# Kernel optimization log

Hardware: AMD Instinct MI355X
Metric: run time of the kernel (lower is better)

Reference implementation:

```python
import jax, jax.numpy as jnp
import numpy as np

N, F, HD, E, K, T, IDX = 50000, 128, 256, 800000, 3, 7, 0


def setup_inputs() -> dict:
    key = jax.random.key(0)
    ks = jax.random.split(key, 18)
    s = 0.05  # param init scale
    return {
        "x": jax.random.normal(ks[0], (N, F), jnp.float32),
        "edge_index": jax.random.randint(ks[1], (2, E), 0, N),
        "edge_weight": jax.random.uniform(ks[2], (E,), jnp.float32),
        "h": jax.random.normal(ks[3], (N, HD), jnp.float32),
        "c": jax.random.normal(ks[4], (N, HD), jnp.float32),
        # 4 ChebConvs on X and 4 on H (gates i, f, c, o), each with K Chebyshev weights
        "theta_x": jax.random.normal(ks[5], (4, K, F, HD), jnp.float32) * s,
        "bias_x": jnp.zeros((4, HD), jnp.float32),
        "theta_h": jax.random.normal(ks[6], (4, K, HD, HD), jnp.float32) * s,
        "bias_h": jnp.zeros((4, HD), jnp.float32),
        "w_c": jax.random.normal(ks[7], (3, HD), jnp.float32) * s,  # peephole w_c_i, w_c_f, w_c_o
        "b_gate": jnp.zeros((4, HD), jnp.float32),  # b_i, b_f, b_c, b_o
        # decoder LSTM (input_size=1, hidden=HD), torch gate order i, f, g, o
        "w_ih": jax.random.normal(ks[8], (4 * HD, 1), jnp.float32) * s,
        "w_hh": jax.random.normal(ks[9], (4 * HD, HD), jnp.float32) * s,
        "b_ih": jnp.zeros((4 * HD,), jnp.float32),
        "b_hh": jnp.zeros((4 * HD,), jnp.float32),
        "w_out": jax.random.normal(ks[10], (1, HD), jnp.float32) * s,
        "b_out": jnp.zeros((1,), jnp.float32),
    }


def _cheb_stack(feat, src, dst, w_norm):
    """Stacked Chebyshev bases [K, N, d]; L_hat = -A_norm (sym norm, lambda_max=2)."""
    def lhat(v):
        msg = w_norm[:, None] * v[src]              # [E, d] gather
        return -jax.ops.segment_sum(msg, dst, num_segments=N)  # scatter-add
    Tx = [feat]
    if K > 1:
        Tx.append(lhat(feat))
    for _ in range(2, K):
        Tx.append(2.0 * lhat(Tx[-1]) - Tx[-2])
    return jnp.stack(Tx)


def reference(x, edge_index, edge_weight, h, c, theta_x, bias_x, theta_h, bias_h,
              w_c, b_gate, w_ih, w_hh, b_ih, b_hh, w_out, b_out):
    src, dst = edge_index[0], edge_index[1]
    # ChebConv.__norm__: remove self loops, sym-normalized Laplacian, scale by 2/lambda_max=1,
    # add -I -> L_hat off-diag = -w_norm, diag = 0
    w = jnp.where(src == dst, 0.0, edge_weight)
    deg = jax.ops.segment_sum(w, src, num_segments=N)
    dis = jnp.where(deg > 0, jax.lax.rsqrt(jnp.maximum(deg, 1e-20)), 0.0)
    w_norm = dis[src] * w * dis[dst]

    # GConvLSTM encode: one conv per gate on X and on H; bases shared across gates
    gx = jnp.einsum('knf,gkfo->gno', _cheb_stack(x, src, dst, w_norm), theta_x) + bias_x[:, None, :]
    gh = jnp.einsum('knf,gkfo->gno', _cheb_stack(h, src, dst, w_norm), theta_h) + bias_h[:, None, :]
    g = gx + gh  # [4, N, HD] gates i, f, c, o
    I = jax.nn.sigmoid(g[0] + w_c[0] * c + b_gate[0])
    Fg = jax.nn.sigmoid(g[1] + w_c[1] * c + b_gate[1])
    Cn = Fg * c + I * jnp.tanh(g[2] + b_gate[2])
    O = jax.nn.sigmoid(g[3] + w_c[2] * Cn + b_gate[3])
    Hn = O * jnp.tanh(Cn)

    h0 = Hn[IDX:IDX + 1]          # [1, HD]
    c0 = Cn[IDX:IDX + 1]
    inp0 = x[IDX, -1:][None]      # [1, 1]

    def step(carry, _):
        hd, cd, inp = carry
        gates = inp @ w_ih.T + hd @ w_hh.T + b_ih + b_hh  # [1, 4*HD]
        i, f, gg, o = jnp.split(gates, 4, axis=1)
        cn = jax.nn.sigmoid(f) * cd + jax.nn.sigmoid(i) * jnp.tanh(gg)
        hn = jax.nn.sigmoid(o) * jnp.tanh(cn)
        out = hn @ w_out.T + b_out                         # [1, 1]
        return (hn, cn, out), out

    _, outs = jax.lax.scan(step, (h0, c0, inp0), None, length=T)  # [T, 1, 1]
    prediction = outs[:, :, 0]  # squeeze dim 2 -> [T, 1]
    return prediction
```

## Files before the change

kernel.cpp:

```cpp
#include <hip/hip_runtime.h>
#include <math.h>

#define NN 50000
#define FD 128
#define HDIM 256
#define NE 800000
#define NBR_CAP 512
#define M_CAP 8192
#define TT 7
#define TPB 256
#define GB 96
#define PSLICE 12
#define GRP 21
#define ECHUNK 2048
#define SBLK 32
#define FGRID (GB + SBLK)
#define SPIN_CAP 50000000

#define O_NBRCNT   0
#define O_MCNT     64
#define O_GDONE    128
#define O_HSYNC    512
#define O_DEG      16896
#define O_BITMAP   216896
#define O_ZERO_END 223168
#define O_NBRNODE  223168
#define O_NBRW     225216
#define O_MS       227264
#define O_MD       260032
#define O_MW       292800
#define O_GPART    325568

__device__ __forceinline__ float sigm(float v) { return 1.f / (1.f + expf(-v)); }
__device__ __forceinline__ float dis_of(float dg) {
    return dg > 0.f ? rsqrtf(fmaxf(dg, 1e-20f)) : 0.f;
}
__device__ __forceinline__ float slf(const float* p) {
    return __hip_atomic_load(p, __ATOMIC_RELAXED, __HIP_MEMORY_SCOPE_SYSTEM);
}
__device__ __forceinline__ void ssf(float* p, float v) {
    __hip_atomic_store(p, v, __ATOMIC_RELAXED, __HIP_MEMORY_SCOPE_SYSTEM);
}

__global__ void k_nbr(const int* __restrict__ ei, const float* __restrict__ ew,
                      char* __restrict__ ws) {
    int*   nbrCnt = (int*)(ws + O_NBRCNT);
    int*   nbrNode= (int*)(ws + O_NBRNODE);
    float* nbrW   = (float*)(ws + O_NBRW);

    int gid = blockIdx.x * blockDim.x + threadIdx.x;
    if (gid < (O_ZERO_END - O_MCNT) / 4) ((unsigned*)(ws + O_MCNT))[gid] = 0u;

    int e0 = gid * 4;
    if (e0 >= NE) return;
    int4 d4 = *(const int4*)&ei[NE + e0];
    float4 w4 = *(const float4*)&ew[e0];
    int dd[4] = {d4.x, d4.y, d4.z, d4.w};
    float wv[4] = {w4.x, w4.y, w4.z, w4.w};
    #pragma unroll
    for (int k = 0; k < 4; ++k) {
        if (dd[k] == 0 && wv[k] != 0.f) {
            int s = ei[e0 + k];
            if (s != 0) {
                int slot = atomicAdd(nbrCnt, 1);
                if (slot < NBR_CAP) { nbrNode[slot] = s; nbrW[slot] = wv[k]; }
            }
        }
    }
}

__global__ void k_match(const int* __restrict__ ei, const float* __restrict__ ew,
                        char* __restrict__ ws) {
    const int* nbrCnt = (const int*)(ws + O_NBRCNT);
    const int* nbrNode= (const int*)(ws + O_NBRNODE);
    int*      mCnt   = (int*)(ws + O_MCNT);
    int*      mS     = (int*)(ws + O_MS);
    int*      mD     = (int*)(ws + O_MD);
    float*    mW     = (float*)(ws + O_MW);
    unsigned* bitmap = (unsigned*)(ws + O_BITMAP);

    __shared__ int sNode[NBR_CAP];
    __shared__ int sCnt;
    if (threadIdx.x == 0) sCnt = min(*nbrCnt, NBR_CAP);
    __syncthreads();
    int cnt = sCnt;
    for (int i = threadIdx.x; i < cnt; i += blockDim.x) sNode[i] = nbrNode[i];
    __syncthreads();
    if (blockIdx.x == 0 && threadIdx.x == 0) atomicOr(&bitmap[0], 1u);

    int i = blockIdx.x * blockDim.x + threadIdx.x;
    int e0 = i * 4;
    if (e0 >= NE) return;
    int4 s4 = *(const int4*)&ei[e0];
    int4 d4 = *(const int4*)&ei[NE + e0];
    float4 w4 = *(const float4*)&ew[e0];
    int ss[4] = {s4.x, s4.y, s4.z, s4.w};
    int dd[4] = {d4.x, d4.y, d4.z, d4.w};
    float wv[4] = {w4.x, w4.y, w4.z, w4.w};
    bool m[4];
    #pragma unroll
    for (int k = 0; k < 4; ++k) m[k] = (dd[k] == 0);
    for (int j = 0; j < cnt; ++j) {
        int nv = sNode[j];
        #pragma unroll
        for (int k = 0; k < 4; ++k) m[k] |= (dd[k] == nv);
    }
    #pragma unroll
    for (int k = 0; k < 4; ++k) {
        int s = ss[k], d = dd[k];
        float w = wv[k];
        if (s == d || w == 0.f || !m[k]) continue;
        int slot = atomicAdd(mCnt, 1);
        if (slot < M_CAP) { mS[slot] = s; mD[slot] = d; mW[slot] = w; }
        atomicOr(&bitmap[s >> 5], 1u << (s & 31));
        atomicOr(&bitmap[d >> 5], 1u << (d & 31));
    }
}

__global__ void k_deg(const int* __restrict__ ei, const float* __restrict__ ew,
                      char* __restrict__ ws) {
    const unsigned* bitmap = (const unsigned*)(ws + O_BITMAP);
    float* deg = (float*)(ws + O_DEG);
    int i = blockIdx.x * blockDim.x + threadIdx.x;
    int e0 = i * 4;
    if (e0 >= NE) return;
    int4 s4 = *(const int4*)&ei[e0];
    int4 d4 = *(const int4*)&ei[NE + e0];
    float4 w4 = *(const float4*)&ew[e0];
    int ss[4] = {s4.x, s4.y, s4.z, s4.w};
    int dd[4] = {d4.x, d4.y, d4.z, d4.w};
    float wv[4] = {w4.x, w4.y, w4.z, w4.w};
    #pragma unroll
    for (int k = 0; k < 4; ++k) {
        int s = ss[k];
        if (s == dd[k] || wv[k] == 0.f) continue;
        if (bitmap[s >> 5] & (1u << (s & 31)))
            atomicAdd(&deg[s], wv[k]);
    }
}

__global__ __launch_bounds__(TPB) void k_fused(
    const float* __restrict__ x, const float* __restrict__ h, const float* __restrict__ c,
    const float* __restrict__ theta_x, const float* __restrict__ bias_x,
    const float* __restrict__ theta_h, const float* __restrict__ bias_h,
    const float* __restrict__ w_c, const float* __restrict__ b_gate,
    const float* __restrict__ w_ih, const float* __restrict__ w_hh,
    const float* __restrict__ b_ih, const float* __restrict__ b_hh,
    const float* __restrict__ w_out, const float* __restrict__ b_out,
    float* __restrict__ out, char* __restrict__ ws) {

    const float*        deg    = (const float*)(ws + O_DEG);
    const int*          nbrCnt = (const int*)(ws + O_NBRCNT);
    const int*          mCnt   = (const int*)(ws + O_MCNT);
    const int*          nbrNode= (const int*)(ws + O_NBRNODE);
    const float*        nbrW   = (const float*)(ws + O_NBRW);
    const int*          mS     = (const int*)(ws + O_MS);
    const int*          mD     = (const int*)(ws + O_MD);
    const float*        mW     = (const float*)(ws + O_MW);
    float*              gpart  = (float*)(ws + O_GPART);
    unsigned*           gdone  = (unsigned*)(ws + O_GDONE);
    unsigned long long* hsync  = (unsigned long long*)(ws + O_HSYNC);

    __shared__ int   sNode[NBR_CAP];
    __shared__ float sWl[NBR_CAP];
    __shared__ float cf1[ECHUNK], cf2[ECHUNK];
    __shared__ int   sS[ECHUNK];
    __shared__ float tp1[GRP][PSLICE], tp2[GRP][PSLICE];
    __shared__ float tslice[PSLICE];
    __shared__ __align__(16) float sh[HDIM];
    __shared__ float sdot[32];
    __shared__ float swsum[4];
    __shared__ int   sCnt, sMcnt;

    const int tid = threadIdx.x, bid = blockIdx.x;

    if (bid < GB) {
        if (tid == 0) { sCnt = min(*nbrCnt, NBR_CAP); sMcnt = min(*mCnt, M_CAP); }
        __syncthreads();
        const int ncnt = sCnt, mcnt = sMcnt;
        for (int i = tid; i < ncnt; i += TPB) { sNode[i] = nbrNode[i]; sWl[i] = nbrW[i]; }
        __syncthreads();

        const bool isx = bid < 32;
        const int qstart = bid * PSLICE - (isx ? 0 : 3 * FD);
        const float* fb0 = isx ? x : h;
        const int fstride = isx ? FD : HDIM;

        const int pl = tid % PSLICE, gr = tid / PSLICE;
        const float* fbase = fb0 + (qstart + pl) % fstride;
        const float dis0 = dis_of(deg[0]);

        float a1 = 0.f, a2 = 0.f;
        for (int c0i = 0; c0i < mcnt; c0i += ECHUNK) {
            int clen = min(ECHUNK, mcnt - c0i);
            for (int i = tid; i < clen; i += TPB) {
                int sI = mS[c0i + i], dI = mD[c0i + i];
                float w = mW[c0i + i];
                float disd = dis_of(deg[dI]);
                float wn = dis_of(deg[sI]) * w * disd;
                float Wd = 0.f;
                for (int j = 0; j < ncnt; ++j) Wd += (sNode[j] == dI) ? sWl[j] : 0.f;
                cf1[i] = (dI == 0) ? wn : 0.f;
                cf2[i] = wn * (dis0 * disd * Wd);
                sS[i] = sI;
            }
            __syncthreads();
            if (gr < GRP) {
                int i = gr;
                for (; i + 3 * GRP < clen; i += 4 * GRP) {
                    int s0 = sS[i], s1 = sS[i + GRP], s2 = sS[i + 2 * GRP], s3 = sS[i + 3 * GRP];
                    float c10 = cf1[i], c11 = cf1[i + GRP], c12 = cf1[i + 2 * GRP], c13 = cf1[i + 3 * GRP];
                    float c20 = cf2[i], c21 = cf2[i + GRP], c22 = cf2[i + 2 * GRP], c23 = cf2[i + 3 * GRP];
                    float v0 = fbase[(size_t)s0 * fstride];
                    float v1 = fbase[(size_t)s1 * fstride];
                    float v2 = fbase[(size_t)s2 * fstride];
                    float v3 = fbase[(size_t)s3 * fstride];
                    a1 += c10 * v0 + c11 * v1 + c12 * v2 + c13 * v3;
                    a2 += c20 * v0 + c21 * v1 + c22 * v2 + c23 * v3;
                }
                for (; i < clen; i += GRP) {
                    float v = fbase[(size_t)sS[i] * fstride];
                    a1 += cf1[i] * v;
                    a2 += cf2[i] * v;
                }
            }
            __syncthreads();
        }
        if (gr < GRP) { tp1[gr][pl] = a1; tp2[gr][pl] = a2; }
        __syncthreads();
        if (tid < PSLICE) {
            float A1 = 0.f, A2 = 0.f;
            #pragma unroll
            for (int g2 = 0; g2 < GRP; ++g2) { A1 += tp1[g2][tid]; A2 += tp2[g2][tid]; }
            int q = qstart + tid;
            int ko = q / fstride;
            float ff0 = fb0[q % fstride];
            tslice[tid] = (ko == 0) ? ff0 : ((ko == 1) ? -A1 : 2.f * A2 - ff0);
        }
        __syncthreads();

        {
            const float* tb = isx ? theta_x : theta_h;
            const size_t gs = isx ? (size_t)(3 * FD) * HDIM : (size_t)(3 * HDIM) * HDIM;
            float g0 = 0.f, g1 = 0.f, g2v = 0.f, g3 = 0.f;
            #pragma unroll
            for (int pp = 0; pp < PSLICE; ++pp) {
                float tv = tslice[pp];
                const float* row = tb + (size_t)(qstart + pp) * HDIM;
                g0  += tv * row[tid];
                g1  += tv * row[gs + tid];
                g2v += tv * row[2 * gs + tid];
                g3  += tv * row[3 * gs + tid];
            }
            float* gp = gpart + (size_t)bid * 1024;
            ssf(&gp[tid], g0);
            ssf(&gp[HDIM + tid], g1);
            ssf(&gp[2 * HDIM + tid], g2v);
            ssf(&gp[3 * HDIM + tid], g3);
        }
        __syncthreads();
        if (tid == 0)
            __hip_atomic_store(&gdone[bid], 1u, __ATOMIC_RELEASE, __HIP_MEMORY_SCOPE_SYSTEM);
        return;
    }

    const int sbid = bid - GB;

    const int rl = tid >> 3, seg = tid & 7;
    const int grow = (rl >> 3) * HDIM + sbid * 8 + (rl & 7);
    float4 wreg[8];
    #pragma unroll
    for (int k = 0; k < 8; ++k)
        wreg[k] = *(const float4*)&w_hh[(size_t)grow * HDIM + seg * 32 + k * 4];
    const float wih_r = w_ih[grow];
    const float br    = b_ih[grow] + b_hh[grow];
    const float bo    = b_out[0];
    const float wout_r = w_out[tid];

    if (tid < GB) {
        int sp = 0;
        while (__hip_atomic_load(&gdone[tid], __ATOMIC_RELAXED,
                                 __HIP_MEMORY_SCOPE_SYSTEM) == 0u) {
            if (++sp > SPIN_CAP) break;
        }
    }
    __syncthreads();

    {
        const int d = tid >> 3, j = tid & 7;
        const int g = d >> 3, kk = d & 7, o = sbid * 8 + kk;
        float s = 0.f;
        #pragma unroll
        for (int pb = j; pb < GB; pb += 8) s += slf(&gpart[(size_t)pb * 1024 + g * HDIM + o]);
        s += __shfl_down(s, 4);
        s += __shfl_down(s, 2);
        s += __shfl_down(s, 1);
        if (j == 0) sdot[d] = s;
    }
    __syncthreads();

    float creg = 0.f;
    if (tid < 8) {
        const int o = sbid * 8 + tid;
        float g0 = sdot[tid]      + bias_x[o]            + bias_h[o];
        float g1 = sdot[8 + tid]  + bias_x[HDIM + o]     + bias_h[HDIM + o];
        float g2 = sdot[16 + tid] + bias_x[2 * HDIM + o] + bias_h[2 * HDIM + o];
        float g3 = sdot[24 + tid] + bias_x[3 * HDIM + o] + bias_h[3 * HDIM + o];
        float c0 = c[o];
        float I  = sigm(g0 + w_c[o] * c0 + b_gate[o]);
        float Fg = sigm(g1 + w_c[HDIM + o] * c0 + b_gate[HDIM + o]);
        float Cn = Fg * c0 + I * tanhf(g2 + b_gate[2 * HDIM + o]);
        float O  = sigm(g3 + w_c[2 * HDIM + o] * Cn + b_gate[3 * HDIM + o]);
        float h0 = O * tanhf(Cn);
        creg = Cn;
        unsigned long long pk = (1ull << 32) | (unsigned long long)__float_as_uint(h0);
        __hip_atomic_store(&hsync[o], pk, __ATOMIC_RELAXED, __HIP_MEMORY_SCOPE_SYSTEM);
    }
    {
        unsigned long long v;
        int sp = 0;
        do {
            v = __hip_atomic_load(&hsync[tid], __ATOMIC_RELAXED, __HIP_MEMORY_SCOPE_SYSTEM);
            if ((unsigned)(v >> 32) == 1u) break;
        } while (++sp < SPIN_CAP);
        sh[tid] = __uint_as_float((unsigned)v);
    }
    __syncthreads();
    float sinp = x[FD - 1];

    for (int t = 0; t < TT; ++t) {
        float acc = 0.f;
        const float* shh = &sh[seg * 32];
        #pragma unroll
        for (int k = 0; k < 8; ++k) {
            float4 hv = *(const float4*)&shh[k * 4];
            acc += hv.x * wreg[k].x + hv.y * wreg[k].y + hv.z * wreg[k].z + hv.w * wreg[k].w;
        }
        acc += __shfl_down(acc, 4);
        acc += __shfl_down(acc, 2);
        acc += __shfl_down(acc, 1);
        if (seg == 0) sdot[rl] = acc + sinp * wih_r + br;
        __syncthreads();
        if (tid < 8) {
            float iv = sdot[tid], fv = sdot[8 + tid], gv = sdot[16 + tid], ov = sdot[24 + tid];
            float cn = sigm(fv) * creg + sigm(iv) * tanhf(gv);
            float hn = sigm(ov) * tanhf(cn);
            creg = cn;
            unsigned long long pk = (((unsigned long long)(t + 2)) << 32)
                                  | (unsigned long long)__float_as_uint(hn);
            __hip_atomic_store(&hsync[(t + 1) * HDIM + sbid * 8 + tid], pk,
                               __ATOMIC_RELAXED, __HIP_MEMORY_SCOPE_SYSTEM);
        }
        float hval;
        {
            unsigned long long v;
            int sp = 0;
            do {
                v = __hip_atomic_load(&hsync[(t + 1) * HDIM + tid],
                                      __ATOMIC_RELAXED, __HIP_MEMORY_SCOPE_SYSTEM);
                if ((unsigned)(v >> 32) == (unsigned)(t + 2)) break;
            } while (++sp < SPIN_CAP);
            hval = __uint_as_float((unsigned)v);
        }
        sh[tid] = hval;
        float pw = wout_r * hval;
        pw += __shfl_down(pw, 32);
        pw += __shfl_down(pw, 16);
        pw += __shfl_down(pw, 8);
        pw += __shfl_down(pw, 4);
        pw += __shfl_down(pw, 2);
        pw += __shfl_down(pw, 1);
        if ((tid & 63) == 0) swsum[tid >> 6] = pw;
        __syncthreads();
        float sval = swsum[0] + swsum[1] + swsum[2] + swsum[3] + bo;
        sinp = sval;
        if (sbid == 0 && tid == 0) out[t] = sval;
    }
}

extern "C" void kernel_launch(void* const* d_in, const int* in_sizes, int n_in,
                              void* d_out, int out_size, void* d_ws, size_t ws_size,
                              hipStream_t stream) {
    const float* x       = (const float*)d_in[0];
    const int*   ei      = (const int*)d_in[1];
    const float* ew      = (const float*)d_in[2];
    const float* h       = (const float*)d_in[3];
    const float* c       = (const float*)d_in[4];
    const float* theta_x = (const float*)d_in[5];
    const float* bias_x  = (const float*)d_in[6];
    const float* theta_h = (const float*)d_in[7];
    const float* bias_h  = (const float*)d_in[8];
    const float* w_c     = (const float*)d_in[9];
    const float* b_gate  = (const float*)d_in[10];
    const float* w_ih    = (const float*)d_in[11];
    const float* w_hh    = (const float*)d_in[12];
    const float* b_ih    = (const float*)d_in[13];
    const float* b_hh    = (const float*)d_in[14];
    const float* w_out   = (const float*)d_in[15];
    const float* b_out   = (const float*)d_in[16];
    char* ws = (char*)d_ws;
    float* out = (float*)d_out;

    hipMemsetAsync(ws, 0, 64, stream);

    int eb4 = (NE / 4 + TPB - 1) / TPB;
    k_nbr<<<eb4, TPB, 0, stream>>>(ei, ew, ws);
    k_match<<<eb4, TPB, 0, stream>>>(ei, ew, ws);
    k_deg<<<eb4, TPB, 0, stream>>>(ei, ew, ws);
    k_fused<<<FGRID, TPB, 0, stream>>>(x, h, c, theta_x, bias_x, theta_h, bias_h,
                                       w_c, b_gate, w_ih, w_hh, b_ih, b_hh,
                                       w_out, b_out, out, ws);
}
```

Measured before the change: 53.62 us.

## Replace in-kernel spin-synchronized LSTM decode with per-step kernel launches

The autoregressive decoder no longer runs inside the fused kernel with cross-block spin-waits on tagged hsync values. The fused kernel now writes the initial h and c to workspace buffers, and a separate small kernel is launched for each of the seven decode steps, followed by a final kernel for the last output. Kernel boundaries replace the global flag polling, removing atomic spinning and the risk of blocks that are not co-resident. The cost is eight extra launches and w_hh being reloaded from memory on every step instead of staying in registers.

```diff
diff --git a/kernel.cpp b/kernel.cpp
--- a/kernel.cpp
+++ b/kernel.cpp
@@ -15,21 +15,23 @@
 #define ECHUNK 2048
 #define SBLK 32
 #define FGRID (GB + SBLK)
+#define SB 32
 #define SPIN_CAP 50000000
 
 #define O_NBRCNT   0
 #define O_MCNT     64
 #define O_GDONE    128
-#define O_HSYNC    512
-#define O_DEG      16896
-#define O_BITMAP   216896
-#define O_ZERO_END 223168
-#define O_NBRNODE  223168
-#define O_NBRW     225216
-#define O_MS       227264
-#define O_MD       260032
-#define O_MW       292800
-#define O_GPART    325568
+#define O_DEG      512
+#define O_BITMAP   200512
+#define O_ZERO_END 206784
+#define O_NBRNODE  206784
+#define O_NBRW     208832
+#define O_MS       210880
+#define O_MD       243648
+#define O_MW       276416
+#define O_GPART    309184
+#define O_HBUF     702400
+#define O_CBUF     710592
 
 __device__ __forceinline__ float sigm(float v) { return 1.f / (1.f + expf(-v)); }
 __device__ __forceinline__ float dis_of(float dg) {
@@ -144,22 +146,20 @@
     const float* __restrict__ theta_x, const float* __restrict__ bias_x,
     const float* __restrict__ theta_h, const float* __restrict__ bias_h,
     const float* __restrict__ w_c, const float* __restrict__ b_gate,
-    const float* __restrict__ w_ih, const float* __restrict__ w_hh,
-    const float* __restrict__ b_ih, const float* __restrict__ b_hh,
-    const float* __restrict__ w_out, const float* __restrict__ b_out,
-    float* __restrict__ out, char* __restrict__ ws) {
-
-    const float*        deg    = (const float*)(ws + O_DEG);
-    const int*          nbrCnt = (const int*)(ws + O_NBRCNT);
-    const int*          mCnt   = (const int*)(ws + O_MCNT);
-    const int*          nbrNode= (const int*)(ws + O_NBRNODE);
-    const float*        nbrW   = (const float*)(ws + O_NBRW);
-    const int*          mS     = (const int*)(ws + O_MS);
-    const int*          mD     = (const int*)(ws + O_MD);
-    const float*        mW     = (const float*)(ws + O_MW);
-    float*              gpart  = (float*)(ws + O_GPART);
-    unsigned*           gdone  = (unsigned*)(ws + O_GDONE);
-    unsigned long long* hsync  = (unsigned long long*)(ws + O_HSYNC);
+    char* __restrict__ ws) {
+
+    const float*  deg    = (const float*)(ws + O_DEG);
+    const int*    nbrCnt = (const int*)(ws + O_NBRCNT);
+    const int*    mCnt   = (const int*)(ws + O_MCNT);
+    const int*    nbrNode= (const int*)(ws + O_NBRNODE);
+    const float*  nbrW   = (const float*)(ws + O_NBRW);
+    const int*    mS     = (const int*)(ws + O_MS);
+    const int*    mD     = (const int*)(ws + O_MD);
+    const float*  mW     = (const float*)(ws + O_MW);
+    float*        gpart  = (float*)(ws + O_GPART);
+    unsigned*     gdone  = (unsigned*)(ws + O_GDONE);
+    float*        hbuf   = (float*)(ws + O_HBUF);
+    float*        cbuf   = (float*)(ws + O_CBUF);
 
     __shared__ int   sNode[NBR_CAP];
     __shared__ float sWl[NBR_CAP];
@@ -167,9 +167,7 @@
     __shared__ int   sS[ECHUNK];
     __shared__ float tp1[GRP][PSLICE], tp2[GRP][PSLICE];
     __shared__ float tslice[PSLICE];
-    __shared__ __align__(16) float sh[HDIM];
     __shared__ float sdot[32];
-    __shared__ float swsum[4];
     __shared__ int   sCnt, sMcnt;
 
     const int tid = threadIdx.x, bid = blockIdx.x;
@@ -266,17 +264,6 @@
 
     const int sbid = bid - GB;
 
-    const int rl = tid >> 3, seg = tid & 7;
-    const int grow = (rl >> 3) * HDIM + sbid * 8 + (rl & 7);
-    float4 wreg[8];
-    #pragma unroll
-    for (int k = 0; k < 8; ++k)
-        wreg[k] = *(const float4*)&w_hh[(size_t)grow * HDIM + seg * 32 + k * 4];
-    const float wih_r = w_ih[grow];
-    const float br    = b_ih[grow] + b_hh[grow];
-    const float bo    = b_out[0];
-    const float wout_r = w_out[tid];
-
     if (tid < GB) {
         int sp = 0;
         while (__hip_atomic_load(&gdone[tid], __ATOMIC_RELAXED,
@@ -299,7 +286,6 @@
     }
     __syncthreads();
 
-    float creg = 0.f;
     if (tid < 8) {
         const int o = sbid * 8 + tid;
         float g0 = sdot[tid]      + bias_x[o]            + bias_h[o];
@@ -311,71 +297,86 @@
         float Fg = sigm(g1 + w_c[HDIM + o] * c0 + b_gate[HDIM + o]);
         float Cn = Fg * c0 + I * tanhf(g2 + b_gate[2 * HDIM + o]);
         float O  = sigm(g3 + w_c[2 * HDIM + o] * Cn + b_gate[3 * HDIM + o]);
-        float h0 = O * tanhf(Cn);
-        creg = Cn;
-        unsigned long long pk = (1ull << 32) | (unsigned long long)__float_as_uint(h0);
-        __hip_atomic_store(&hsync[o], pk, __ATOMIC_RELAXED, __HIP_MEMORY_SCOPE_SYSTEM);
-    }
-    {
-        unsigned long long v;
-        int sp = 0;
-        do {
-            v = __hip_atomic_load(&hsync[tid], __ATOMIC_RELAXED, __HIP_MEMORY_SCOPE_SYSTEM);
-            if ((unsigned)(v >> 32) == 1u) break;
-        } while (++sp < SPIN_CAP);
-        sh[tid] = __uint_as_float((unsigned)v);
-    }
-    __syncthreads();
-    float sinp = x[FD - 1];
-
-    for (int t = 0; t < TT; ++t) {
-        float acc = 0.f;
-        const float* shh = &sh[seg * 32];
-        #pragma unroll
-        for (int k = 0; k < 8; ++k) {
-            float4 hv = *(const float4*)&shh[k * 4];
-            acc += hv.x * wreg[k].x + hv.y * wreg[k].y + hv.z * wreg[k].z + hv.w * wreg[k].w;
-        }
-        acc += __shfl_down(acc, 4);
-        acc += __shfl_down(acc, 2);
-        acc += __shfl_down(acc, 1);
-        if (seg == 0) sdot[rl] = acc + sinp * wih_r + br;
-        __syncthreads();
-        if (tid < 8) {
-            float iv = sdot[tid], fv = sdot[8 + tid], gv = sdot[16 + tid], ov = sdot[24 + tid];
-            float cn = sigm(fv) * creg + sigm(iv) * tanhf(gv);
-            float hn = sigm(ov) * tanhf(cn);
-            creg = cn;
-            unsigned long long pk = (((unsigned long long)(t + 2)) << 32)
-                                  | (unsigned long long)__float_as_uint(hn);
-            __hip_atomic_store(&hsync[(t + 1) * HDIM + sbid * 8 + tid], pk,
-                               __ATOMIC_RELAXED, __HIP_MEMORY_SCOPE_SYSTEM);
-        }
-        float hval;
-        {
-            unsigned long long v;
-            int sp = 0;
-            do {
-                v = __hip_atomic_load(&hsync[(t + 1) * HDIM + tid],
-                                      __ATOMIC_RELAXED, __HIP_MEMORY_SCOPE_SYSTEM);
-                if ((unsigned)(v >> 32) == (unsigned)(t + 2)) break;
-            } while (++sp < SPIN_CAP);
-            hval = __uint_as_float((unsigned)v);
-        }
-        sh[tid] = hval;
-        float pw = wout_r * hval;
-        pw += __shfl_down(pw, 32);
-        pw += __shfl_down(pw, 16);
-        pw += __shfl_down(pw, 8);
-        pw += __shfl_down(pw, 4);
-        pw += __shfl_down(pw, 2);
-        pw += __shfl_down(pw, 1);
-        if ((tid & 63) == 0) swsum[tid >> 6] = pw;
-        __syncthreads();
-        float sval = swsum[0] + swsum[1] + swsum[2] + swsum[3] + bo;
-        sinp = sval;
-        if (sbid == 0 && tid == 0) out[t] = sval;
-    }
+        hbuf[o] = O * tanhf(Cn);
+        cbuf[o] = Cn;
+    }
+}
+
+__global__ __launch_bounds__(TPB) void k_step(
+    int t, const float* __restrict__ x,
+    const float* __restrict__ w_ih, const float* __restrict__ w_hh,
+    const float* __restrict__ b_ih, const float* __restrict__ b_hh,
+    const float* __restrict__ w_out, const float* __restrict__ b_out,
+    float* __restrict__ out, char* __restrict__ ws) {
+
+    float* hbuf = (float*)(ws + O_HBUF);
+    float* cbuf = (float*)(ws + O_CBUF);
+
+    __shared__ __align__(16) float sh[HDIM];
+    __shared__ float sdot[32];
+    __shared__ float swsum[4];
+
+    const int tid = threadIdx.x, bid = blockIdx.x;
+    const float* hr = hbuf + t * HDIM;
+
+    float hv = hr[tid];
+    sh[tid] = hv;
+    float pw = hv * w_out[tid];
+    pw += __shfl_down(pw, 32);
+    pw += __shfl_down(pw, 16);
+    pw += __shfl_down(pw, 8);
+    pw += __shfl_down(pw, 4);
+    pw += __shfl_down(pw, 2);
+    pw += __shfl_down(pw, 1);
+    if ((tid & 63) == 0) swsum[tid >> 6] = pw;
+    __syncthreads();
+    const float bo = b_out[0];
+    const float sval = swsum[0] + swsum[1] + swsum[2] + swsum[3] + bo;
+    const float sinp = (t == 0) ? x[FD - 1] : sval;
+    if (t > 0 && bid == 0 && tid == 0) out[t - 1] = sval;
+
+    const int rl = tid >> 3, seg = tid & 7;
+    const int grow = (rl >> 3) * HDIM + bid * 8 + (rl & 7);
+    const float* wrow = w_hh + (size_t)grow * HDIM + seg * 32;
+    const float* shh = &sh[seg * 32];
+    float acc = 0.f;
+    #pragma unroll
+    for (int k = 0; k < 8; ++k) {
+        float4 wv = *(const float4*)&wrow[k * 4];
+        float4 hv4 = *(const float4*)&shh[k * 4];
+        acc += hv4.x * wv.x + hv4.y * wv.y + hv4.z * wv.z + hv4.w * wv.w;
+    }
+    acc += __shfl_down(acc, 4);
+    acc += __shfl_down(acc, 2);
+    acc += __shfl_down(acc, 1);
+    if (seg == 0) sdot[rl] = acc + sinp * w_ih[grow] + b_ih[grow] + b_hh[grow];
+    __syncthreads();
+
+    if (tid < 8) {
+        const int dim = bid * 8 + tid;
+        float cd = cbuf[t * HDIM + dim];
+        float iv = sdot[tid], fv = sdot[8 + tid], gv = sdot[16 + tid], ov = sdot[24 + tid];
+        float cn = sigm(fv) * cd + sigm(iv) * tanhf(gv);
+        float hn = sigm(ov) * tanhf(cn);
+        hbuf[(t + 1) * HDIM + dim] = hn;
+        cbuf[(t + 1) * HDIM + dim] = cn;
+    }
+}
+
+__global__ void k_fin(const float* __restrict__ w_out, const float* __restrict__ b_out,
+                      float* __restrict__ out, char* __restrict__ ws) {
+    const float* hr = (const float*)(ws + O_HBUF) + TT * HDIM;
+    const int tid = threadIdx.x;
+    float pw = 0.f;
+    #pragma unroll
+    for (int j = 0; j < 4; ++j) pw += hr[tid * 4 + j] * w_out[tid * 4 + j];
+    pw += __shfl_down(pw, 32);
+    pw += __shfl_down(pw, 16);
+    pw += __shfl_down(pw, 8);
+    pw += __shfl_down(pw, 4);
+    pw += __shfl_down(pw, 2);
+    pw += __shfl_down(pw, 1);
+    if (tid == 0) out[TT - 1] = pw + b_out[0];
 }
 
 extern "C" void kernel_launch(void* const* d_in, const int* in_sizes, int n_in,
@@ -408,6 +409,8 @@
     k_match<<<eb4, TPB, 0, stream>>>(ei, ew, ws);
     k_deg<<<eb4, TPB, 0, stream>>>(ei, ew, ws);
     k_fused<<<FGRID, TPB, 0, stream>>>(x, h, c, theta_x, bias_x, theta_h, bias_h,
-                                       w_c, b_gate, w_ih, w_hh, b_ih, b_hh,
-                                       w_out, b_out, out, ws);
-}
+                                       w_c, b_gate, ws);
+    for (int t = 0; t < TT; ++t)
+        k_step<<<SB, TPB, 0, stream>>>(t, x, w_ih, w_hh, b_ih, b_hh, w_out, b_out, out, ws);
+    k_fin<<<1, 64, 0, stream>>>(w_out, b_out, out, ws);
+}
```

New measurement: 66.62 us. 1.24x slower.

## Split decoder LSTM tail into separate kernel, replacing initial hsync handoff

Applied to the files above, without the earlier changes.

The autoregressive decoder is moved out of the fused kernel into a new k_tail2 launch of 32 blocks. The fused kernel now writes the initial h and c state to global buffers instead of publishing h through the spin-synchronised hsync slots. This drops one cross-block spin barrier and the w_hh register preload from the fused kernel, so those blocks finish sooner. In exchange it adds a kernel launch boundary, and the tail can no longer preload its weights while the gate-partial blocks are still working.

```diff
diff --git a/kernel.cpp b/kernel.cpp
--- a/kernel.cpp
+++ b/kernel.cpp
@@ -15,31 +15,34 @@
 #define ECHUNK 2048
 #define SBLK 32
 #define FGRID (GB + SBLK)
+#define SB 32
 #define SPIN_CAP 50000000
 
 #define O_NBRCNT   0
 #define O_MCNT     64
 #define O_GDONE    128
 #define O_HSYNC    512
-#define O_DEG      16896
-#define O_BITMAP   216896
-#define O_ZERO_END 223168
-#define O_NBRNODE  223168
-#define O_NBRW     225216
-#define O_MS       227264
-#define O_MD       260032
-#define O_MW       292800
-#define O_GPART    325568
+#define O_HBUF     16896
+#define O_CBUF     17920
+#define O_DEG      18944
+#define O_BITMAP   218944
+#define O_ZERO_END 225216
+#define O_NBRNODE  225216
+#define O_NBRW     227264
+#define O_MS       229312
+#define O_MD       262080
+#define O_MW       294848
+#define O_GPART    327616
 
 __device__ __forceinline__ float sigm(float v) { return 1.f / (1.f + expf(-v)); }
 __device__ __forceinline__ float dis_of(float dg) {
     return dg > 0.f ? rsqrtf(fmaxf(dg, 1e-20f)) : 0.f;
 }
+__device__ __forceinline__ void ssf(float* p, float v) {
+    __hip_atomic_store(p, v, __ATOMIC_RELAXED, __HIP_MEMORY_SCOPE_SYSTEM);
+}
 __device__ __forceinline__ float slf(const float* p) {
     return __hip_atomic_load(p, __ATOMIC_RELAXED, __HIP_MEMORY_SCOPE_SYSTEM);
-}
-__device__ __forceinline__ void ssf(float* p, float v) {
-    __hip_atomic_store(p, v, __ATOMIC_RELAXED, __HIP_MEMORY_SCOPE_SYSTEM);
 }
 
 __global__ void k_nbr(const int* __restrict__ ei, const float* __restrict__ ew,
@@ -144,22 +147,20 @@
     const float* __restrict__ theta_x, const float* __restrict__ bias_x,
     const float* __restrict__ theta_h, const float* __restrict__ bias_h,
     const float* __restrict__ w_c, const float* __restrict__ b_gate,
-    const float* __restrict__ w_ih, const float* __restrict__ w_hh,
-    const float* __restrict__ b_ih, const float* __restrict__ b_hh,
-    const float* __restrict__ w_out, const float* __restrict__ b_out,
-    float* __restrict__ out, char* __restrict__ ws) {
-
-    const float*        deg    = (const float*)(ws + O_DEG);
-    const int*          nbrCnt = (const int*)(ws + O_NBRCNT);
-    const int*          mCnt   = (const int*)(ws + O_MCNT);
-    const int*          nbrNode= (const int*)(ws + O_NBRNODE);
-    const float*        nbrW   = (const float*)(ws + O_NBRW);
-    const int*          mS     = (const int*)(ws + O_MS);
-    const int*          mD     = (const int*)(ws + O_MD);
-    const float*        mW     = (const float*)(ws + O_MW);
-    float*              gpart  = (float*)(ws + O_GPART);
-    unsigned*           gdone  = (unsigned*)(ws + O_GDONE);
-    unsigned long long* hsync  = (unsigned long long*)(ws + O_HSYNC);
+    char* __restrict__ ws) {
+
+    const float*  deg    = (const float*)(ws + O_DEG);
+    const int*    nbrCnt = (const int*)(ws + O_NBRCNT);
+    const int*    mCnt   = (const int*)(ws + O_MCNT);
+    const int*    nbrNode= (const int*)(ws + O_NBRNODE);
+    const float*  nbrW   = (const float*)(ws + O_NBRW);
+    const int*    mS     = (const int*)(ws + O_MS);
+    const int*    mD     = (const int*)(ws + O_MD);
+    const float*  mW     = (const float*)(ws + O_MW);
+    float*        gpart  = (float*)(ws + O_GPART);
+    unsigned*     gdone  = (unsigned*)(ws + O_GDONE);
+    float*        hbuf   = (float*)(ws + O_HBUF);
+    float*        cbuf   = (float*)(ws + O_CBUF);
 
     __shared__ int   sNode[NBR_CAP];
     __shared__ float sWl[NBR_CAP];
@@ -167,9 +168,7 @@
     __shared__ int   sS[ECHUNK];
     __shared__ float tp1[GRP][PSLICE], tp2[GRP][PSLICE];
     __shared__ float tslice[PSLICE];
-    __shared__ __align__(16) float sh[HDIM];
     __shared__ float sdot[32];
-    __shared__ float swsum[4];
     __shared__ int   sCnt, sMcnt;
 
     const int tid = threadIdx.x, bid = blockIdx.x;
@@ -266,17 +265,6 @@
 
     const int sbid = bid - GB;
 
-    const int rl = tid >> 3, seg = tid & 7;
-    const int grow = (rl >> 3) * HDIM + sbid * 8 + (rl & 7);
-    float4 wreg[8];
-    #pragma unroll
-    for (int k = 0; k < 8; ++k)
-        wreg[k] = *(const float4*)&w_hh[(size_t)grow * HDIM + seg * 32 + k * 4];
-    const float wih_r = w_ih[grow];
-    const float br    = b_ih[grow] + b_hh[grow];
-    const float bo    = b_out[0];
-    const float wout_r = w_out[tid];
-
     if (tid < GB) {
         int sp = 0;
         while (__hip_atomic_load(&gdone[tid], __ATOMIC_RELAXED,
@@ -299,7 +287,6 @@
     }
     __syncthreads();
 
-    float creg = 0.f;
     if (tid < 8) {
         const int o = sbid * 8 + tid;
         float g0 = sdot[tid]      + bias_x[o]            + bias_h[o];
@@ -311,20 +298,41 @@
         float Fg = sigm(g1 + w_c[HDIM + o] * c0 + b_gate[HDIM + o]);
         float Cn = Fg * c0 + I * tanhf(g2 + b_gate[2 * HDIM + o]);
         float O  = sigm(g3 + w_c[2 * HDIM + o] * Cn + b_gate[3 * HDIM + o]);
-        float h0 = O * tanhf(Cn);
-        creg = Cn;
-        unsigned long long pk = (1ull << 32) | (unsigned long long)__float_as_uint(h0);
-        __hip_atomic_store(&hsync[o], pk, __ATOMIC_RELAXED, __HIP_MEMORY_SCOPE_SYSTEM);
-    }
-    {
-        unsigned long long v;
-        int sp = 0;
-        do {
-            v = __hip_atomic_load(&hsync[tid], __ATOMIC_RELAXED, __HIP_MEMORY_SCOPE_SYSTEM);
-            if ((unsigned)(v >> 32) == 1u) break;
-        } while (++sp < SPIN_CAP);
-        sh[tid] = __uint_as_float((unsigned)v);
-    }
+        hbuf[o] = O * tanhf(Cn);
+        cbuf[o] = Cn;
+    }
+}
+
+__global__ __launch_bounds__(TPB) void k_tail2(
+    const float* __restrict__ x,
+    const float* __restrict__ w_ih, const float* __restrict__ w_hh,
+    const float* __restrict__ b_ih, const float* __restrict__ b_hh,
+    const float* __restrict__ w_out, const float* __restrict__ b_out,
+    float* __restrict__ out, char* __restrict__ ws) {
+
+    unsigned long long* hsync = (unsigned long long*)(ws + O_HSYNC);
+    const float* hbuf = (const float*)(ws + O_HBUF);
+    const float* cbuf = (const float*)(ws + O_CBUF);
+
+    __shared__ __align__(16) float sh[HDIM];
+    __shared__ float sdot[32];
+    __shared__ float swsum[4];
+
+    const int tid = threadIdx.x, bid = blockIdx.x;
+
+    const int rl = tid >> 3, seg = tid & 7;
+    const int grow = (rl >> 3) * HDIM + bid * 8 + (rl & 7);
+    float4 wreg[8];
+    #pragma unroll
+    for (int k = 0; k < 8; ++k)
+        wreg[k] = *(const float4*)&w_hh[(size_t)grow * HDIM + seg * 32 + k * 4];
+    const float wih_r = w_ih[grow];
+    const float br    = b_ih[grow] + b_hh[grow];
+    const float bo    = b_out[0];
+    const float wout_r = w_out[tid];
+
+    sh[tid] = hbuf[tid];
+    float creg = (tid < 8) ? cbuf[bid * 8 + tid] : 0.f;
     __syncthreads();
     float sinp = x[FD - 1];
 
@@ -348,7 +356,7 @@
             creg = cn;
             unsigned long long pk = (((unsigned long long)(t + 2)) << 32)
                                   | (unsigned long long)__float_as_uint(hn);
-            __hip_atomic_store(&hsync[(t + 1) * HDIM + sbid * 8 + tid], pk,
+            __hip_atomic_store(&hsync[(t + 1) * HDIM + bid * 8 + tid], pk,
                                __ATOMIC_RELAXED, __HIP_MEMORY_SCOPE_SYSTEM);
         }
         float hval;
@@ -374,7 +382,7 @@
         __syncthreads();
         float sval = swsum[0] + swsum[1] + swsum[2] + swsum[3] + bo;
         sinp = sval;
-        if (sbid == 0 && tid == 0) out[t] = sval;
+        if (bid == 0 && tid == 0) out[t] = sval;
     }
 }
 
@@ -408,6 +416,6 @@
     k_match<<<eb4, TPB, 0, stream>>>(ei, ew, ws);
     k_deg<<<eb4, TPB, 0, stream>>>(ei, ew, ws);
     k_fused<<<FGRID, TPB, 0, stream>>>(x, h, c, theta_x, bias_x, theta_h, bias_h,
-                                       w_c, b_gate, w_ih, w_hh, b_ih, b_hh,
-                                       w_out, b_out, out, ws);
-}
+                                       w_c, b_gate, ws);
+    k_tail2<<<SB, TPB, 0, stream>>>(x, w_ih, w_hh, b_ih, b_hh, w_out, b_out, out, ws);
+}
```

Measured after the change: 54.84 us. 1.02x slower.
